# Kernel tuning notes

Measured on AMD Instinct MI355X. Metric: run time of the kernel, lower is better.

## Reference

```python
import jax, jax.numpy as jnp
import numpy as np

GNN_NODES = 100000
D = 256          # hidden_channels / embed_dim
T = 4096         # tgt_len
B = 64           # bsz


def setup_inputs() -> dict:
    key = jax.random.key(0)
    k1, k2, k3, k4, k5, k6 = jax.random.split(key, 6)
    batch_nodes = jax.random.randint(k1, (B, T), 0, GNN_NODES, dtype=jnp.int64)
    batch_nodes_exe = jax.random.randint(k2, (B, T), 0, 2, dtype=jnp.int32)
    src = jax.random.normal(k3, (T, B, D), dtype=jnp.float32)
    # precomputed GNN node embeddings (self.graph_dict, detached)
    graph_dict = jax.random.normal(k4, (GNN_NODES, D), dtype=jnp.float32)
    # linear0 params
    W0 = jax.random.normal(k5, (D, D), dtype=jnp.float32) / np.sqrt(D)
    b0 = jax.random.normal(k6, (D,), dtype=jnp.float32) * 0.01
    return {"batch_nodes": batch_nodes, "batch_nodes_exe": batch_nodes_exe,
            "src": src, "graph_dict": graph_dict, "W0": W0, "b0": b0}


def reference(batch_nodes, batch_nodes_exe, src, graph_dict, W0, b0):
    tgt_len, bsz, embed_dim = src.shape
    # Vectorized last-occurrence-of-1 search (replaces the Python loop):
    pos = jnp.arange(tgt_len, dtype=jnp.int32)                      # [T]
    masked_pos = jnp.where(batch_nodes_exe == 1, pos[None, :], -1)  # [B,T]
    doc_id = jnp.max(masked_pos, axis=1)                            # [B], -1 if no 1
    has_one = doc_id >= 0                                           # [B]
    safe_doc = jnp.clip(doc_id, 0, tgt_len - 1)
    node_idx = jnp.take_along_axis(batch_nodes, safe_doc[:, None].astype(batch_nodes.dtype), axis=1)[:, 0]  # [B]
    gathered = graph_dict[node_idx]                                 # [B,D]
    new_x = jnp.where(has_one[:, None], gathered, 0.0)[:, None, :]  # [B,1,D]
    gate_x = has_one.astype(src.dtype)[:, None]                     # [B,1]
    # linear0
    x = jnp.einsum('bod,ed->boe', new_x, W0) + b0                   # [B,1,D]
    # scaled similarity: [B,1,D] @ [B,D,T] -> [B,1,T]
    scale = 1.0 / jnp.sqrt(jnp.asarray(embed_dim, dtype=jnp.float32))
    cosine_sim_matrix = jnp.einsum('bod,tbd->bot', x, src) * scale
    return (cosine_sim_matrix, gate_x)
```

## Files before the change

kernel.cpp:

```cpp
#include <hip/hip_runtime.h>

#define T 4096
#define B 64
#define D 256

__global__ __launch_bounds__(256) void prep_kernel(
    const int* __restrict__ batch_nodes, const int* __restrict__ exe,
    const float* __restrict__ graph_dict, const float* __restrict__ W0,
    const float* __restrict__ b0, float* __restrict__ x_ws,
    float* __restrict__ gate_out)
{
    const int b   = blockIdx.x;
    const int tid = threadIdx.x;

    int best = -1;
    const int* erow = exe + (size_t)b * T;
    for (int t = tid; t < T; t += 256)
        if (erow[t] == 1) best = t;

    for (int off = 32; off > 0; off >>= 1) {
        int o = __shfl_down(best, off, 64);
        best = best > o ? best : o;
    }
    __shared__ int sred[4];
    __shared__ int s_doc;
    const int wid = tid >> 6, lane = tid & 63;
    if (lane == 0) sred[wid] = best;
    __syncthreads();
    if (tid == 0) {
        int m = sred[0];
        if (sred[1] > m) m = sred[1];
        if (sred[2] > m) m = sred[2];
        if (sred[3] > m) m = sred[3];
        s_doc = m;
    }
    __syncthreads();

    const int  doc  = s_doc;
    const bool has  = doc >= 0;
    const int  safe = has ? doc : 0;
    const int  node = batch_nodes[(size_t)b * T + safe];

    __shared__ float s_g[D];
    s_g[tid] = has ? graph_dict[(size_t)node * D + tid] : 0.0f;
    __syncthreads();

    const int e = tid;
    const float4* wrow = (const float4*)(W0 + (size_t)e * D);
    float acc = b0[e];
    #pragma unroll 8
    for (int d4 = 0; d4 < D / 4; ++d4) {
        float4 w = wrow[d4];
        acc += s_g[d4 * 4 + 0] * w.x + s_g[d4 * 4 + 1] * w.y
             + s_g[d4 * 4 + 2] * w.z + s_g[d4 * 4 + 3] * w.w;
    }
    x_ws[(size_t)b * D + e] = acc;
    if (tid == 0) gate_out[b] = has ? 1.0f : 0.0f;
}

__global__ __launch_bounds__(256) void sim_kernel(
    const float* __restrict__ src, const float* __restrict__ x_ws,
    float* __restrict__ out)
{
    const int t    = blockIdx.x;
    const int wave = threadIdx.x >> 6;
    const int lane = threadIdx.x & 63;
    const int b0   = wave * 16;

    const float* srow = src  + (size_t)t * (B * D) + (size_t)b0 * D + lane * 4;
    const float* xrow = x_ws + (size_t)b0 * D + lane * 4;

    float res = 0.0f;
    #pragma unroll
    for (int i = 0; i < 16; ++i) {
        const float4 sv = *(const float4*)(srow + i * D);
        const float4 xv = *(const float4*)(xrow + i * D);
        float a = sv.x * xv.x + sv.y * xv.y + sv.z * xv.z + sv.w * xv.w;
        a += __shfl_xor(a, 1, 64);
        a += __shfl_xor(a, 2, 64);
        a += __shfl_xor(a, 4, 64);
        a += __shfl_xor(a, 8, 64);
        a += __shfl_xor(a, 16, 64);
        a += __shfl_xor(a, 32, 64);
        if (lane == i) res = a;
    }
    if (lane < 16)
        out[(size_t)(b0 + lane) * T + t] = res * 0.0625f;
}

extern "C" void kernel_launch(void* const* d_in, const int* in_sizes, int n_in,
                              void* d_out, int out_size, void* d_ws, size_t ws_size,
                              hipStream_t stream) {
    const int*   batch_nodes = (const int*)d_in[0];
    const int*   exe         = (const int*)d_in[1];
    const float* src         = (const float*)d_in[2];
    const float* graph_dict  = (const float*)d_in[3];
    const float* W0          = (const float*)d_in[4];
    const float* b0          = (const float*)d_in[5];

    float* out  = (float*)d_out;
    float* gate = out + (size_t)B * T;
    float* x_ws = (float*)d_ws;

    prep_kernel<<<B, 256, 0, stream>>>(batch_nodes, exe, graph_dict, W0, b0, x_ws, gate);
    sim_kernel<<<T, 256, 0, stream>>>(src, x_ws, out);
}
```

Baseline: 410.5 us.

## Use transpose-style shuffle reduction and process four timesteps per block

Each wave in the similarity kernel now does a butterfly transpose-reduction over its 16 dot products. This replaces 16 separate six-step shuffle reductions with roughly 17 shuffles in total, cutting cross-lane traffic. Each block now handles four consecutive timesteps and writes them as one float4 per batch row, which coalesces output stores and quarters the grid. The prep kernel also reads the exe mask as int4. The trade-off is more registers per thread and lane-index bookkeeping that must be exactly right for correctness.

Result: no change. 408.1 us (-0.6%).

```diff
diff --git a/kernel.cpp b/kernel.cpp
--- a/kernel.cpp
+++ b/kernel.cpp
@@ -14,9 +14,15 @@
     const int tid = threadIdx.x;
 
     int best = -1;
-    const int* erow = exe + (size_t)b * T;
-    for (int t = tid; t < T; t += 256)
-        if (erow[t] == 1) best = t;
+    const int4* erow4 = (const int4*)(exe + (size_t)b * T);
+    for (int q = tid; q < T / 4; q += 256) {
+        int4 v = erow4[q];
+        const int t = q * 4;
+        if (v.x == 1) best = t;
+        if (v.y == 1) best = t + 1;
+        if (v.z == 1) best = t + 2;
+        if (v.w == 1) best = t + 3;
+    }
 
     for (int off = 32; off > 0; off >>= 1) {
         int o = __shfl_down(best, off, 64);
@@ -62,30 +68,71 @@
     const float* __restrict__ src, const float* __restrict__ x_ws,
     float* __restrict__ out)
 {
-    const int t    = blockIdx.x;
     const int wave = threadIdx.x >> 6;
     const int lane = threadIdx.x & 63;
     const int b0   = wave * 16;
+    const int t0   = blockIdx.x * 4;
 
-    const float* srow = src  + (size_t)t * (B * D) + (size_t)b0 * D + lane * 4;
     const float* xrow = x_ws + (size_t)b0 * D + lane * 4;
 
-    float res = 0.0f;
+    float resk[4];
     #pragma unroll
-    for (int i = 0; i < 16; ++i) {
-        const float4 sv = *(const float4*)(srow + i * D);
-        const float4 xv = *(const float4*)(xrow + i * D);
-        float a = sv.x * xv.x + sv.y * xv.y + sv.z * xv.z + sv.w * xv.w;
-        a += __shfl_xor(a, 1, 64);
-        a += __shfl_xor(a, 2, 64);
-        a += __shfl_xor(a, 4, 64);
-        a += __shfl_xor(a, 8, 64);
-        a += __shfl_xor(a, 16, 64);
-        a += __shfl_xor(a, 32, 64);
-        if (lane == i) res = a;
+    for (int k = 0; k < 4; ++k) {
+        const int t = t0 + k;
+        const float* srow = src + (size_t)t * (B * D) + (size_t)b0 * D + lane * 4;
+
+        float a[16];
+        #pragma unroll
+        for (int i = 0; i < 16; ++i) {
+            const float4 sv = *(const float4*)(srow + i * D);
+            const float4 xv = *(const float4*)(xrow + i * D);
+            a[i] = sv.x * xv.x + sv.y * xv.y + sv.z * xv.z + sv.w * xv.w;
+        }
+
+        float v8[8];
+        #pragma unroll
+        for (int j = 0; j < 8; ++j) {
+            const float xx = a[2 * j], yy = a[2 * j + 1];
+            const float send = (lane & 1) ? xx : yy;
+            const float recv = __shfl_xor(send, 1, 64);
+            v8[j] = ((lane & 1) ? yy : xx) + recv;
+        }
+        float v4a[4];
+        #pragma unroll
+        for (int j = 0; j < 4; ++j) {
+            const float xx = v8[2 * j], yy = v8[2 * j + 1];
+            const float send = (lane & 2) ? xx : yy;
+            const float recv = __shfl_xor(send, 2, 64);
+            v4a[j] = ((lane & 2) ? yy : xx) + recv;
+        }
+        float v2a[2];
+        #pragma unroll
+        for (int j = 0; j < 2; ++j) {
+            const float xx = v4a[2 * j], yy = v4a[2 * j + 1];
+            const float send = (lane & 4) ? xx : yy;
+            const float recv = __shfl_xor(send, 4, 64);
+            v2a[j] = ((lane & 4) ? yy : xx) + recv;
+        }
+        float v1;
+        {
+            const float xx = v2a[0], yy = v2a[1];
+            const float send = (lane & 8) ? xx : yy;
+            const float recv = __shfl_xor(send, 8, 64);
+            v1 = ((lane & 8) ? yy : xx) + recv;
+        }
+        v1 += __shfl_xor(v1, 16, 64);
+        v1 += __shfl_xor(v1, 32, 64);
+        resk[k] = v1;
     }
-    if (lane < 16)
-        out[(size_t)(b0 + lane) * T + t] = res * 0.0625f;
+
+    if (lane < 16) {
+        float4 o;
+        o.x = resk[0] * 0.0625f;
+        o.y = resk[1] * 0.0625f;
+        o.z = resk[2] * 0.0625f;
+        o.w = resk[3] * 0.0625f;
+        *(float4*)(out + (size_t)(b0 + lane) * T + t0) = o;
+    }
 }
 
 extern "C" void kernel_launch(void* const* d_in, const int* in_sizes, int n_in,
@@ -103,5 +150,5 @@
     float* x_ws = (float*)d_ws;
 
     prep_kernel<<<B, 256, 0, stream>>>(batch_nodes, exe, graph_dict, W0, b0, x_ws, gate);
-    sim_kernel<<<T, 256, 0, stream>>>(src, x_ws, out);
+    sim_kernel<<<T / 4, 256, 0, stream>>>(src, x_ws, out);
 }
```
